# Kernel tuning notes

Measured on AMD Instinct MI355X. Metric: run time of the kernel, lower is better.

## Reference

```python
import jax, jax.numpy as jnp
import numpy as np


def setup_inputs() -> dict:
    key = jax.random.key(0)
    ks = jax.random.split(key, 7)
    B, N, K, D = 256, 50, 12, 128
    return {
        "batch_size": B,
        "itm_emb": jax.random.normal(ks[0], (B, N, D), jnp.float32),
        "ave_sess_itms_emb": jax.random.normal(ks[1], (B, N, D), jnp.float32),
        "glob_adj_itm_embs": jax.random.normal(ks[2], (B, N, K, D), jnp.float32),
        "glob_adj_wgt_embs": jax.random.normal(ks[3], (B, N, K), jnp.float32),
        "w1": jax.random.normal(ks[4], (D + 1, D), jnp.float32) * 0.1,
        "w2": jax.random.normal(ks[5], (D, 1), jnp.float32) * 0.1,
        "w3": jax.random.normal(ks[6], (2 * D, D), jnp.float32) * 0.1,
    }


def reference(batch_size, itm_emb, ave_sess_itms_emb, glob_adj_itm_embs,
              glob_adj_wgt_embs, w1, w2, w3):
    D = itm_emb.shape[-1]
    # [B,N,1,D] * [B,N,K,D] -> [B,N,K,D]; concat weight -> [B,N,K,D+1]
    alpha = ave_sess_itms_emb[:, :, None, :] * glob_adj_itm_embs
    alpha = jnp.concatenate([alpha, glob_adj_wgt_embs[..., None]], axis=-1)
    alpha = jnp.einsum('bnkc,cd->bnkd', alpha, w1)          # [B,N,K,D]
    alpha = jax.nn.leaky_relu(alpha, negative_slope=0.2)
    alpha = jnp.einsum('bnkd,do->bnk', alpha, w2)           # [B,N,K]
    alpha = jax.nn.softmax(alpha, axis=-1)[..., None]       # [B,N,K,1]
    att = jnp.sum(alpha * glob_adj_itm_embs, axis=-2)       # [B,N,D]
    g = jnp.concatenate([itm_emb, att], axis=-1)            # [B,N,2D]
    # dropout with p=0.0 / eval mode is identity
    g = jnp.einsum('bnc,cd->bnd', g, w3)
    g = g.reshape(batch_size, -1, D)
    return jax.nn.relu(g)
```

## Files before the change

kernel.cpp:

```cpp
#include <hip/hip_runtime.h>

#define DD 128
#define KADJ 12
#define BN_TOTAL 12800

typedef float f32x4 __attribute__((ext_vector_type(4)));
typedef float f32x2 __attribute__((ext_vector_type(2)));
typedef __bf16 bf16x8 __attribute__((ext_vector_type(8)));
typedef unsigned int u32;

__device__ __forceinline__ bf16x8 cvt8(f32x4 a, f32x4 b) {
    bf16x8 r;
    r[0] = (__bf16)a[0]; r[1] = (__bf16)a[1]; r[2] = (__bf16)a[2]; r[3] = (__bf16)a[3];
    r[4] = (__bf16)b[0]; r[5] = (__bf16)b[1]; r[6] = (__bf16)b[2]; r[7] = (__bf16)b[3];
    return r;
}

__global__ void k_prep(const float* __restrict__ w1, const float* __restrict__ w3,
                       __bf16* __restrict__ w1f, __bf16* __restrict__ w3f) {
    int idx = blockIdx.x * 256 + threadIdx.x;
    int lane = (idx >> 3) & 63, e = idx & 7;
    int l = lane & 15, gg = lane >> 4;
    if (idx < 16384) {
        int fi = idx >> 9, n = fi >> 2, ks = fi & 3;
        int k = ks * 32 + gg * 8 + e;
        w1f[idx] = (__bf16)w1[k * DD + n * 16 + l];
    } else {
        int j = idx - 16384;
        int fi = j >> 9, n = fi >> 3, ks = fi & 7;
        int k = ks * 32 + gg * 8 + e;
        w3f[j] = (__bf16)w3[k * DD + n * 16 + l];
    }
}

__launch_bounds__(256, 4)
__global__ void k_att(const float* __restrict__ ave, const float* __restrict__ adj,
                      const float* __restrict__ wgt, const float* __restrict__ w1,
                      const float* __restrict__ w2, const __bf16* __restrict__ w1f,
                      float* __restrict__ att_out) {
    __shared__ unsigned char lds[2 * 48 * 256 + 48 * 4];
    unsigned char* Ab   = lds;
    unsigned char* adjb = lds + 12288;
    float* sco = (float*)(lds + 24576);

    const int t = threadIdx.x;
    const int lane = t & 63;
    const int w = t >> 6;
    const int l = lane & 15, g = lane >> 4;
    const int Bn0 = blockIdx.x * 4;
    const size_t R0 = (size_t)Bn0 * KADJ;

    #pragma unroll
    for (int i = 0; i < 3; ++i) {
        int idx = i * 256 + t;
        int row = idx >> 4, c8 = idx & 15;
        int bl = row / 12;
        const float* gs = adj + (R0 + row) * (size_t)DD + c8 * 8;
        f32x4 v0 = *reinterpret_cast<const f32x4*>(gs);
        f32x4 v1 = *reinterpret_cast<const f32x4*>(gs + 4);
        const float* as = ave + (size_t)(Bn0 + bl) * DD + c8 * 8;
        f32x4 e0 = *reinterpret_cast<const f32x4*>(as);
        f32x4 e1 = *reinterpret_cast<const f32x4*>(as + 4);
        int off = row * 256 + ((c8 ^ (row & 15)) << 4);
        *reinterpret_cast<bf16x8*>(adjb + off) = cvt8(v0, v1);
        *reinterpret_cast<bf16x8*>(Ab + off)   = cvt8(v0 * e0, v1 * e1);
    }
    __syncthreads();

    if (w < 3) {
        const int lr = w * 16 + l;
        f32x4 acc[8];
        #pragma unroll
        for (int n = 0; n < 8; ++n) acc[n] = f32x4{0.f, 0.f, 0.f, 0.f};
        #pragma unroll 1
        for (int ks = 0; ks < 4; ++ks) {
            bf16x8 bq[8];
            #pragma unroll
            for (int n = 0; n < 8; ++n)
                bq[n] = *reinterpret_cast<const bf16x8*>(
                    w1f + ((size_t)(n * 4 + ks) * 512 + lane * 8));
            bf16x8 af = *reinterpret_cast<const bf16x8*>(
                Ab + lr * 256 + (((ks * 4 + g) ^ (lr & 15)) << 4));
            #pragma unroll
            for (int n = 0; n < 8; ++n)
                acc[n] = __builtin_amdgcn_mfma_f32_16x16x32_bf16(af, bq[n], acc[n], 0, 0, 0);
        }
        float wv[4];
        #pragma unroll
        for (int j = 0; j < 4; ++j)
            wv[j] = wgt[R0 + (size_t)w * 16 + g * 4 + j];
        float p[4] = {0.f, 0.f, 0.f, 0.f};
        #pragma unroll
        for (int n = 0; n < 8; ++n) {
            float w1rn = w1[128 * DD + n * 16 + l];
            float w2vn = w2[n * 16 + l];
            #pragma unroll
            for (int j = 0; j < 4; ++j) {
                float h = fmaf(wv[j], w1rn, acc[n][j]);
                h = h > 0.f ? h : 0.2f * h;
                p[j] = fmaf(h, w2vn, p[j]);
            }
        }
        #pragma unroll
        for (int j = 0; j < 4; ++j) {
            p[j] += __shfl_xor(p[j], 1, 64);
            p[j] += __shfl_xor(p[j], 2, 64);
            p[j] += __shfl_xor(p[j], 4, 64);
            p[j] += __shfl_xor(p[j], 8, 64);
        }
        if (l == 0)
            *reinterpret_cast<f32x4*>(&sco[w * 16 + g * 4]) =
                f32x4{p[0], p[1], p[2], p[3]};
    }
    __syncthreads();

    {
        float s[KADJ];
        float mx = -1e30f;
        #pragma unroll
        for (int k = 0; k < KADJ; ++k) { s[k] = sco[w * 12 + k]; mx = fmaxf(mx, s[k]); }
        float ssum = 0.f;
        #pragma unroll
        for (int k = 0; k < KADJ; ++k) { s[k] = __expf(s[k] - mx); ssum += s[k]; }
        float inv = 1.f / ssum;
        float a0 = 0.f, a1 = 0.f;
        #pragma unroll
        for (int k = 0; k < KADJ; ++k) {
            int row = w * 12 + k;
            u32 pk = *reinterpret_cast<const u32*>(
                adjb + row * 256 + (((lane >> 2) ^ (row & 15)) << 4) + (lane & 3) * 4);
            float alpha = s[k] * inv;
            float e0 = __builtin_bit_cast(float, pk << 16);
            float e1 = __builtin_bit_cast(float, pk & 0xFFFF0000u);
            a0 = fmaf(alpha, e0, a0);
            a1 = fmaf(alpha, e1, a1);
        }
        *reinterpret_cast<f32x2*>(att_out + (size_t)(Bn0 + w) * DD + lane * 2) =
            f32x2{a0, a1};
    }
}

__launch_bounds__(256)
__global__ void k_out(const float* __restrict__ itm, const float* att,
                      const __bf16* __restrict__ w3f, float* outp) {
    const int t = threadIdx.x;
    const int lane = t & 63;
    const int w = t >> 6;
    const int l = lane & 15, g = lane >> 4;
    const int R0 = blockIdx.x * 64 + w * 16;
    const int row = R0 + l;

    bf16x8 afr[8];
    const float* ip = itm + (size_t)row * DD;
    #pragma unroll
    for (int s = 0; s < 4; ++s) {
        int c = s * 32 + g * 8;
        f32x4 a0 = *reinterpret_cast<const f32x4*>(ip + c);
        f32x4 a1 = *reinterpret_cast<const f32x4*>(ip + c + 4);
        afr[s] = cvt8(a0, a1);
    }
    const float* ap = att + (size_t)row * DD;
    #pragma unroll
    for (int s = 0; s < 4; ++s) {
        int c = s * 32 + g * 8;
        f32x4 a0 = *reinterpret_cast<const f32x4*>(ap + c);
        f32x4 a1 = *reinterpret_cast<const f32x4*>(ap + c + 4);
        afr[4 + s] = cvt8(a0, a1);
    }

    f32x4 acc[8];
    #pragma unroll
    for (int n = 0; n < 8; ++n) acc[n] = f32x4{0.f, 0.f, 0.f, 0.f};
    #pragma unroll
    for (int s = 0; s < 8; ++s) {
        const __bf16* bp = w3f + ((size_t)s * 64 + lane) * 8;
        #pragma unroll
        for (int n = 0; n < 8; ++n) {
            bf16x8 bfr = *reinterpret_cast<const bf16x8*>(bp + (size_t)n * 4096);
            acc[n] = __builtin_amdgcn_mfma_f32_16x16x32_bf16(afr[s], bfr, acc[n], 0, 0, 0);
        }
    }

    #pragma unroll
    for (int n = 0; n < 8; ++n) {
        #pragma unroll
        for (int j = 0; j < 4; ++j)
            outp[(size_t)(R0 + g * 4 + j) * DD + n * 16 + l] = fmaxf(acc[n][j], 0.f);
    }
}

extern "C" void kernel_launch(void* const* d_in, const int* in_sizes, int n_in,
                              void* d_out, int out_size, void* d_ws, size_t ws_size,
                              hipStream_t stream) {
    const float* itm = (const float*)d_in[1];
    const float* ave = (const float*)d_in[2];
    const float* adj = (const float*)d_in[3];
    const float* wgt = (const float*)d_in[4];
    const float* w1  = (const float*)d_in[5];
    const float* w2  = (const float*)d_in[6];
    const float* w3  = (const float*)d_in[7];
    float* outp = (float*)d_out;

    __bf16* w1f = (__bf16*)d_ws;
    __bf16* w3f = (__bf16*)((char*)d_ws + 32 * 1024);

    k_prep<<<dim3(192), dim3(256), 0, stream>>>(w1, w3, w1f, w3f);
    k_att<<<dim3(BN_TOTAL / 4), dim3(256), 0, stream>>>(ave, adj, wgt, w1, w2, w1f, outp);
    k_out<<<dim3(BN_TOTAL / 64), dim3(256), 0, stream>>>(itm, outp, w3f, outp);
}
```

Baseline: 46.77 us.

## Make attention kernel one-wave-per-item without LDS staging or block barriers

Each wave now handles one (b,n) item. It loads the adjacency rows directly from global memory into MFMA A fragments, padding rows 12-15 by repeating the last row. Softmax is done entirely with cross-lane shuffles instead of LDS scores and __syncthreads, and the weighted sum re-reads adj in fp32 from global/cache. This removes the shared-memory staging and the two block barriers. In exchange, each 16-row MFMA tile wastes 4 rows, and adj is read twice from global memory instead of once.

New measurement: 59.08 us. 26.3% more time.

```diff
diff --git a/kernel.cpp b/kernel.cpp
--- a/kernel.cpp
+++ b/kernel.cpp
@@ -38,106 +38,92 @@
                       const float* __restrict__ wgt, const float* __restrict__ w1,
                       const float* __restrict__ w2, const __bf16* __restrict__ w1f,
                       float* __restrict__ att_out) {
-    __shared__ unsigned char lds[2 * 48 * 256 + 48 * 4];
-    unsigned char* Ab   = lds;
-    unsigned char* adjb = lds + 12288;
-    float* sco = (float*)(lds + 24576);
+    const int lane = threadIdx.x & 63;
+    const int w = threadIdx.x >> 6;
+    const int bn = blockIdx.x * 4 + w;
+    const int l = lane & 15, g = lane >> 4;
+    const int l2 = l < KADJ ? l : KADJ - 1;
 
-    const int t = threadIdx.x;
-    const int lane = t & 63;
-    const int w = t >> 6;
-    const int l = lane & 15, g = lane >> 4;
-    const int Bn0 = blockIdx.x * 4;
-    const size_t R0 = (size_t)Bn0 * KADJ;
+    const float* adjr = adj + (size_t)bn * (KADJ * DD) + (size_t)l2 * DD;
+    const float* aver = ave + (size_t)bn * DD;
 
+    f32x4 acc[8];
     #pragma unroll
-    for (int i = 0; i < 3; ++i) {
-        int idx = i * 256 + t;
-        int row = idx >> 4, c8 = idx & 15;
-        int bl = row / 12;
-        const float* gs = adj + (R0 + row) * (size_t)DD + c8 * 8;
-        f32x4 v0 = *reinterpret_cast<const f32x4*>(gs);
-        f32x4 v1 = *reinterpret_cast<const f32x4*>(gs + 4);
-        const float* as = ave + (size_t)(Bn0 + bl) * DD + c8 * 8;
-        f32x4 e0 = *reinterpret_cast<const f32x4*>(as);
-        f32x4 e1 = *reinterpret_cast<const f32x4*>(as + 4);
-        int off = row * 256 + ((c8 ^ (row & 15)) << 4);
-        *reinterpret_cast<bf16x8*>(adjb + off) = cvt8(v0, v1);
-        *reinterpret_cast<bf16x8*>(Ab + off)   = cvt8(v0 * e0, v1 * e1);
+    for (int n = 0; n < 8; ++n) acc[n] = f32x4{0.f, 0.f, 0.f, 0.f};
+    #pragma unroll 1
+    for (int ks = 0; ks < 4; ++ks) {
+        int c = ks * 32 + g * 8;
+        f32x4 u0 = *reinterpret_cast<const f32x4*>(adjr + c);
+        f32x4 u1 = *reinterpret_cast<const f32x4*>(adjr + c + 4);
+        f32x4 e0 = *reinterpret_cast<const f32x4*>(aver + c);
+        f32x4 e1 = *reinterpret_cast<const f32x4*>(aver + c + 4);
+        bf16x8 af = cvt8(u0 * e0, u1 * e1);
+        bf16x8 bq[8];
+        #pragma unroll
+        for (int n = 0; n < 8; ++n)
+            bq[n] = *reinterpret_cast<const bf16x8*>(
+                w1f + ((size_t)(n * 4 + ks) * 512 + lane * 8));
+        #pragma unroll
+        for (int n = 0; n < 8; ++n)
+            acc[n] = __builtin_amdgcn_mfma_f32_16x16x32_bf16(af, bq[n], acc[n], 0, 0, 0);
     }
-    __syncthreads();
 
-    if (w < 3) {
-        const int lr = w * 16 + l;
-        f32x4 acc[8];
-        #pragma unroll
-        for (int n = 0; n < 8; ++n) acc[n] = f32x4{0.f, 0.f, 0.f, 0.f};
-        #pragma unroll 1
-        for (int ks = 0; ks < 4; ++ks) {
-            bf16x8 bq[8];
-            #pragma unroll
-            for (int n = 0; n < 8; ++n)
-                bq[n] = *reinterpret_cast<const bf16x8*>(
-                    w1f + ((size_t)(n * 4 + ks) * 512 + lane * 8));
-            bf16x8 af = *reinterpret_cast<const bf16x8*>(
-                Ab + lr * 256 + (((ks * 4 + g) ^ (lr & 15)) << 4));
-            #pragma unroll
-            for (int n = 0; n < 8; ++n)
-                acc[n] = __builtin_amdgcn_mfma_f32_16x16x32_bf16(af, bq[n], acc[n], 0, 0, 0);
-        }
-        float wv[4];
-        #pragma unroll
-        for (int j = 0; j < 4; ++j)
-            wv[j] = wgt[R0 + (size_t)w * 16 + g * 4 + j];
-        float p[4] = {0.f, 0.f, 0.f, 0.f};
-        #pragma unroll
-        for (int n = 0; n < 8; ++n) {
-            float w1rn = w1[128 * DD + n * 16 + l];
-            float w2vn = w2[n * 16 + l];
-            #pragma unroll
-            for (int j = 0; j < 4; ++j) {
-                float h = fmaf(wv[j], w1rn, acc[n][j]);
-                h = h > 0.f ? h : 0.2f * h;
-                p[j] = fmaf(h, w2vn, p[j]);
-            }
-        }
+    float wv[4];
+    #pragma unroll
+    for (int j = 0; j < 4; ++j)
+        wv[j] = (g < 3) ? wgt[(size_t)bn * KADJ + g * 4 + j] : 0.f;
+    float p[4] = {0.f, 0.f, 0.f, 0.f};
+    #pragma unroll
+    for (int n = 0; n < 8; ++n) {
+        float w1rn = w1[128 * DD + n * 16 + l];
+        float w2vn = w2[n * 16 + l];
         #pragma unroll
         for (int j = 0; j < 4; ++j) {
-            p[j] += __shfl_xor(p[j], 1, 64);
-            p[j] += __shfl_xor(p[j], 2, 64);
-            p[j] += __shfl_xor(p[j], 4, 64);
-            p[j] += __shfl_xor(p[j], 8, 64);
+            float h = fmaf(wv[j], w1rn, acc[n][j]);
+            h = h > 0.f ? h : 0.2f * h;
+            p[j] = fmaf(h, w2vn, p[j]);
         }
-        if (l == 0)
-            *reinterpret_cast<f32x4*>(&sco[w * 16 + g * 4]) =
-                f32x4{p[0], p[1], p[2], p[3]};
     }
-    __syncthreads();
+    #pragma unroll
+    for (int j = 0; j < 4; ++j) {
+        p[j] += __shfl_xor(p[j], 1, 64);
+        p[j] += __shfl_xor(p[j], 2, 64);
+        p[j] += __shfl_xor(p[j], 4, 64);
+        p[j] += __shfl_xor(p[j], 8, 64);
+        if (g == 3) p[j] = -1e30f;
+    }
 
-    {
-        float s[KADJ];
-        float mx = -1e30f;
-        #pragma unroll
-        for (int k = 0; k < KADJ; ++k) { s[k] = sco[w * 12 + k]; mx = fmaxf(mx, s[k]); }
-        float ssum = 0.f;
-        #pragma unroll
-        for (int k = 0; k < KADJ; ++k) { s[k] = __expf(s[k] - mx); ssum += s[k]; }
-        float inv = 1.f / ssum;
-        float a0 = 0.f, a1 = 0.f;
-        #pragma unroll
-        for (int k = 0; k < KADJ; ++k) {
-            int row = w * 12 + k;
-            u32 pk = *reinterpret_cast<const u32*>(
-                adjb + row * 256 + (((lane >> 2) ^ (row & 15)) << 4) + (lane & 3) * 4);
-            float alpha = s[k] * inv;
-            float e0 = __builtin_bit_cast(float, pk << 16);
-            float e1 = __builtin_bit_cast(float, pk & 0xFFFF0000u);
-            a0 = fmaf(alpha, e0, a0);
-            a1 = fmaf(alpha, e1, a1);
-        }
-        *reinterpret_cast<f32x2*>(att_out + (size_t)(Bn0 + w) * DD + lane * 2) =
-            f32x2{a0, a1};
+    float q0[4], q1[4], q2[4];
+    #pragma unroll
+    for (int j = 0; j < 4; ++j) {
+        q0[j] = __shfl_xor(p[j], 16, 64);
+        q1[j] = __shfl_xor(p[j], 32, 64);
+        q2[j] = __shfl_xor(q1[j], 16, 64);
     }
+    float mx = -1e30f;
+    #pragma unroll
+    for (int j = 0; j < 4; ++j)
+        mx = fmaxf(mx, fmaxf(fmaxf(p[j], q0[j]), fmaxf(q1[j], q2[j])));
+    float ssum = 0.f;
+    #pragma unroll
+    for (int j = 0; j < 4; ++j) {
+        ssum += __expf(p[j] - mx);  ssum += __expf(q0[j] - mx);
+        ssum += __expf(q1[j] - mx); ssum += __expf(q2[j] - mx);
+    }
+    float inv = 1.f / ssum;
+
+    const float* adjp = adj + (size_t)bn * (KADJ * DD);
+    float a0 = 0.f, a1 = 0.f;
+    #pragma unroll
+    for (int k = 0; k < KADJ; ++k) {
+        int d = (k >> 2) ^ g, j = k & 3;
+        float sv = (d == 0) ? p[j] : (d == 1) ? q0[j] : (d == 2) ? q1[j] : q2[j];
+        float alpha = __expf(sv - mx) * inv;
+        a0 = fmaf(alpha, adjp[k * DD + lane], a0);
+        a1 = fmaf(alpha, adjp[k * DD + 64 + lane], a1);
+    }
+    att_out[(size_t)bn * DD + lane] = a0;
+    att_out[(size_t)bn * DD + 64 + lane] = a1;
 }
 
 __launch_bounds__(256)
```
